# Performance work log

Measured on AMD Instinct MI355X. Metric: run time of the kernel, lower is better.

Reference implementation:

```python
import math
import jax, jax.numpy as jnp
import numpy as np

WS = 8      # window_size
NT = 16     # n_theta
NR = 8      # n_r
PD = 32     # polar_proj_dim


def _polar_grid():
    # Matches LocalPolarPrior._build_polar_grid: [NR, NT, 2] with (x, y) in [-1, 1]
    radius = jnp.linspace(0.0, 1.0, NR)
    theta = jnp.linspace(0.0, 2.0 * math.pi, NT + 1)[:-1]
    rr, tt = jnp.meshgrid(radius, theta, indexing='ij')
    return jnp.stack([rr * jnp.cos(tt), rr * jnp.sin(tt)], axis=-1)


def _bilinear_weights():
    # Precompute flat gather indices + weights for F.grid_sample(mode='bilinear',
    # padding_mode='zeros', align_corners=True) on a fixed WSxWS input.
    g = _polar_grid()                                   # [NR, NT, 2]
    px = (g[..., 0] + 1.0) * 0.5 * (WS - 1)             # x -> pixel coords
    py = (g[..., 1] + 1.0) * 0.5 * (WS - 1)
    x0 = jnp.floor(px); y0 = jnp.floor(py)
    wx = px - x0; wy = py - y0
    xs = jnp.stack([x0, x0 + 1, x0, x0 + 1], axis=-1)   # [NR, NT, 4]
    ys = jnp.stack([y0, y0, y0 + 1, y0 + 1], axis=-1)
    ws = jnp.stack([(1 - wx) * (1 - wy), wx * (1 - wy),
                    (1 - wx) * wy, wx * wy], axis=-1)
    valid = (xs >= 0) & (xs < WS) & (ys >= 0) & (ys < WS)
    xi = jnp.clip(xs, 0, WS - 1).astype(jnp.int32)
    yi = jnp.clip(ys, 0, WS - 1).astype(jnp.int32)
    idx = (yi * WS + xi).reshape(NR * NT, 4)            # flat [0, 64)
    wt = (ws * valid).reshape(NR * NT, 4).astype(jnp.float32)
    return idx, wt


def setup_inputs() -> dict:
    key = jax.random.key(0)
    k1, k2, k3 = jax.random.split(key, 3)
    x = jax.random.normal(k1, (8, 96, 384, 384), jnp.float32)
    W_proj = jax.random.normal(k2, (PD, 96), jnp.float32) * 0.1
    b_proj = jax.random.normal(k3, (PD,), jnp.float32) * 0.1
    return {"x": x, "W_proj": W_proj, "b_proj": b_proj}


def reference(x, W_proj, b_proj):
    B, C, H, W = x.shape
    hg, wg = H // WS, W // WS
    # 1x1 conv projection
    feat = jnp.einsum('bchw,oc->bohw', x, W_proj) + b_proj[None, :, None, None]
    # window partition -> [B*hg*wg, PD, WS, WS]
    win = (feat.reshape(B, PD, hg, WS, wg, WS)
               .transpose(0, 2, 4, 1, 3, 5)
               .reshape(B * hg * wg, PD, WS, WS))
    # per-window orthonormal FFT2, shift, log-magnitude
    spec = jnp.fft.fftshift(jnp.fft.fft2(win, norm='ortho'), axes=(-2, -1))
    mag = jnp.log1p(jnp.abs(spec))                      # [N, PD, WS, WS]
    # fixed bilinear polar resample (data-independent weights)
    idx, wt = _bilinear_weights()                       # [NR*NT, 4]
    magf = mag.reshape(-1, PD, WS * WS)
    samp = magf[:, :, idx]                              # [N, PD, NR*NT, 4]
    polar = (samp * wt).sum(-1).reshape(-1, PD, NR, NT)
    # direction distribution per window
    logits = polar.mean(axis=(1, 2))                    # [N, NT]
    dist = jax.nn.softmax(logits, axis=-1)
    d_local = dist.reshape(B, hg, wg, NT).transpose(0, 3, 1, 2)
    entropy = -(d_local * jnp.log(jnp.clip(d_local, 1e-8))).sum(axis=1, keepdims=True)
    confidence = jnp.clip(1.0 - entropy / math.log(NT), 0.0, 1.0)
    return d_local.astype(x.dtype), confidence.astype(x.dtype)
```

## Files before the change

### kernel.cpp

```cpp
#include <hip/hip_runtime.h>
#include <hip/hip_bf16.h>
#include <math.h>

#define NT 16
#define NR 8
#define PD 32
#define HG 48
#define WG 48
#define NB 8
#define CH 96
#define HW 384
#define XHW (HW * HW)
#define S8 0.70710678118654752f

typedef short short8 __attribute__((ext_vector_type(8)));
typedef float f32x4 __attribute__((ext_vector_type(4)));

static __device__ const float CT16[16] = {
    1.0f, 0.9238795325112867f, 0.7071067811865476f, 0.3826834323650898f,
    0.0f, -0.3826834323650898f, -0.7071067811865476f, -0.9238795325112867f,
    -1.0f, -0.9238795325112867f, -0.7071067811865476f, -0.3826834323650898f,
    0.0f, 0.3826834323650898f, 0.7071067811865476f, 0.9238795325112867f};
static __device__ const float ST16[16] = {
    0.0f, 0.3826834323650898f, 0.7071067811865476f, 0.9238795325112867f,
    1.0f, 0.9238795325112867f, 0.7071067811865476f, 0.3826834323650898f,
    0.0f, -0.3826834323650898f, -0.7071067811865476f, -0.9238795325112867f,
    -1.0f, -0.9238795325112867f, -0.7071067811865476f, -0.3826834323650898f};

static __device__ __forceinline__ unsigned short f2bf(float f) {
  unsigned int u = __float_as_uint(f);
  u = u + 0x7fffu + ((u >> 16) & 1u);
  return (unsigned short)(u >> 16);
}
static __device__ __forceinline__ unsigned int pk2bf(float a, float b) {
  union { __hip_bfloat162 h; unsigned int u; } c;
  c.h = __float22bfloat162_rn(make_float2(a, b));
  return c.u;
}
static __device__ __forceinline__ float bf2f_lo(unsigned int v) {
  return __uint_as_float(v << 16);
}
static __device__ __forceinline__ float bf2f_hi(unsigned int v) {
  return __uint_as_float(v & 0xffff0000u);
}

#define MAGR(x_) log1pf(0.125f * fabsf(x_))
#define MAGC(re_, im_) log1pf(0.125f * sqrtf((re_) * (re_) + (im_) * (im_)))

__global__ void lpp_setup(const float* __restrict__ Wp,
                          unsigned short* __restrict__ ws) {
  int gt = blockIdx.x * 256 + threadIdx.x;
  if (gt < 384) {
    int f = gt >> 6, l = gt & 63;
    int ks = f >> 1, nt = f & 1;
    int n = nt * 16 + (l & 15);
    int kbase = ks * 32 + (l >> 4) * 8;
    for (int jj = 0; jj < 8; ++jj)
      ws[(f * 64 + l) * 8 + jj] = f2bf(Wp[n * CH + kbase + jj]);
  }
  if (gt >= 1024 && gt < 2048) {
    int q = gt - 1024;
    int j = q >> 4, t = q & 15;
    float g = 0.f;
    for (int r = 0; r < 8; ++r) {
      float rad = (float)r / 7.0f;
      float px = (rad * CT16[t] + 1.0f) * 3.5f;
      float py = (rad * ST16[t] + 1.0f) * 3.5f;
      float xf = floorf(px), yf = floorf(py);
      float wx = px - xf, wy = py - yf;
      int ix = (int)xf, iy = (int)yf;
      int xi0 = min(max(ix, 0), 7), xi1 = min(max(ix + 1, 0), 7);
      int yi0 = min(max(iy, 0), 7), yi1 = min(max(iy + 1, 0), 7);
      bool vx0 = (ix >= 0) && (ix < 8), vx1 = (ix + 1 >= 0) && (ix + 1 < 8);
      bool vy0 = (iy >= 0) && (iy < 8), vy1 = (iy + 1 >= 0) && (iy + 1 < 8);
      float w0 = (vx0 && vy0) ? (1.f - wx) * (1.f - wy) : 0.f;
      float w1 = (vx1 && vy0) ? wx * (1.f - wy) : 0.f;
      float w2 = (vx0 && vy1) ? (1.f - wx) * wy : 0.f;
      float w3 = (vx1 && vy1) ? wx * wy : 0.f;
      if (yi0 * 8 + xi0 == j) g += w0;
      if (yi0 * 8 + xi1 == j) g += w1;
      if (yi1 * 8 + xi0 == j) g += w2;
      if (yi1 * 8 + xi1 == j) g += w3;
    }
    int f = j >> 5, kc = (j >> 3) & 3, jj = j & 7;
    int l = (kc << 4) | t;
    ws[3072 + (f * 64 + l) * 8 + jj] = f2bf(g);
  }
}

__global__ __launch_bounds__(256, 4) void lpp_main(
    const float* __restrict__ x, const float* __restrict__ bp,
    const unsigned short* __restrict__ ws, float* __restrict__ out) {
  __shared__ short8 ldsX[2048];
  __shared__ float obuf[144];
  unsigned int* ldsU = (unsigned int*)ldsX;

  const int tid = threadIdx.x;
  const int lane = tid & 63;
  const int wave = tid >> 6;
  const int gid = blockIdx.x;
  const int wxg = gid % 6;
  const int hy = (gid / 6) % HG;
  const int b = gid / (6 * HG);
  const short8* wsV = (const short8*)ws;

  f32x4 acc[8][2];
#pragma unroll
  for (int m = 0; m < 8; ++m) {
    acc[m][0] = (f32x4){0.f, 0.f, 0.f, 0.f};
    acc[m][1] = (f32x4){0.f, 0.f, 0.f, 0.f};
  }

  const size_t xcb = (size_t)b * CH * XHW;
  const int kcA = lane >> 4;
  for (int ks = 0; ks < 3; ++ks) {
    if (ks) __syncthreads();
#pragma unroll
    for (int g2 = 0; g2 < 2; ++g2) {
      int id = tid + 256 * g2;
      int kc = id >> 7;
      int p0 = (id & 127) << 2;
      int row = (p0 >> 3) & 7;
      int gcol = wxg * 64 + ((p0 >> 6) << 3) + (p0 & 7);
      const float* xp = x + xcb + (size_t)(ks * 32 + kc * 8) * XHW +
                        (size_t)(hy * 8 + row) * HW + gcol;
      float q[8][4];
#pragma unroll
      for (int jj = 0; jj < 8; ++jj) {
        float4 v = *(const float4*)(xp + (size_t)jj * XHW);
        q[jj][0] = v.x; q[jj][1] = v.y; q[jj][2] = v.z; q[jj][3] = v.w;
      }
      int z = (p0 >> 3) & 7;
      int base3 = kc * 512 + (p0 & ~7);
#pragma unroll
      for (int i = 0; i < 4; ++i) {
        union { unsigned int u[4]; short8 v; } pk;
#pragma unroll
        for (int k2 = 0; k2 < 4; ++k2)
          pk.u[k2] = pk2bf(q[2 * k2][i], q[2 * k2 + 1][i]);
        int u = base3 | ((((p0 & 4) | i)) ^ z);
        ldsX[u] = pk.v;
      }
    }
    __syncthreads();
    short8 b0 = wsV[(ks * 2 + 0) * 64 + lane];
    short8 b1 = wsV[(ks * 2 + 1) * 64 + lane];
    int prow = wave * 128 + (lane & 15);
#pragma unroll
    for (int m = 0; m < 8; ++m) {
      int p = prow + m * 16;
      int s = kcA * 512 + p;
      short8 a = ldsX[s ^ ((p >> 3) & 7)];
      acc[m][0] = __builtin_amdgcn_mfma_f32_16x16x32_bf16(a, b0, acc[m][0], 0, 0, 0);
      acc[m][1] = __builtin_amdgcn_mfma_f32_16x16x32_bf16(a, b1, acc[m][1], 0, 0, 0);
    }
  }
  __syncthreads();

  {
    const float bias0 = bp[lane & 15];
    const float bias1 = bp[16 + (lane & 15)];
    int jb = (lane >> 4) << 2;
#pragma unroll
    for (int m = 0; m < 8; ++m) {
      int win = 2 * wave + (m >> 2);
      int j0 = ((m & 3) << 4) + jb;
#pragma unroll
      for (int nt = 0; nt < 2; ++nt) {
        int p = win * 32 + nt * 16 + (lane & 15);
        float bs = nt ? bias1 : bias0;
        int sh = (p & 15) << 1;
        int dwb = p * 32;
        unsigned int w0 = pk2bf(acc[m][nt][0] + bs, acc[m][nt][1] + bs);
        unsigned int w1 = pk2bf(acc[m][nt][2] + bs, acc[m][nt][3] + bs);
        ldsU[dwb + ((j0 >> 1) ^ sh)] = w0;
        ldsU[dwb + (((j0 >> 1) + 1) ^ sh)] = w1;
      }
    }
  }
  __syncthreads();

  {
    const int p = tid;
    const int sh = (p & 15) << 1;
    const int dwb = p * 32;
    float rr[8][8];
#pragma unroll
    for (int k = 0; k < 8; ++k) {
      float v[8];
#pragma unroll
      for (int i = 0; i < 4; ++i) {
        unsigned int u = ldsU[dwb + ((k * 4 + i) ^ sh)];
        v[2 * i] = bf2f_lo(u);
        v[2 * i + 1] = bf2f_hi(u);
      }
      float a0 = v[0] + v[4], a1 = v[0] - v[4], a2 = v[2] + v[6], a3 = v[2] - v[6];
      float b0 = v[1] + v[5], b1 = v[1] - v[5], b2 = v[3] + v[7], b3 = v[3] - v[7];
      float e0 = a0 + a2, e2 = a0 - a2, o0 = b0 + b2, o2 = b0 - b2;
      float t1 = S8 * (b1 - b3), t2 = S8 * (b1 + b3);
      rr[k][0] = e0 + o0; rr[k][1] = e0 - o0;
      rr[k][2] = a1 + t1; rr[k][3] = -a3 - t2;
      rr[k][4] = e2;      rr[k][5] = -o2;
      rr[k][6] = a1 - t1; rr[k][7] = a3 - t2;
    }
    float mg0[5], mg4[5], mg1[8], mg2[8], mg3[8];
#define REALCOL(SLOT, OUT)                                                    \
  {                                                                           \
    float a0 = rr[0][SLOT] + rr[4][SLOT], a1 = rr[0][SLOT] - rr[4][SLOT];     \
    float a2 = rr[2][SLOT] + rr[6][SLOT], a3 = rr[2][SLOT] - rr[6][SLOT];     \
    float b0 = rr[1][SLOT] + rr[5][SLOT], b1 = rr[1][SLOT] - rr[5][SLOT];     \
    float b2 = rr[3][SLOT] + rr[7][SLOT], b3 = rr[3][SLOT] - rr[7][SLOT];     \
    float e0 = a0 + a2, e2 = a0 - a2, o0 = b0 + b2, o2 = b0 - b2;             \
    float t1 = S8 * (b1 - b3), t2 = S8 * (b1 + b3);                           \
    OUT[0] = MAGR(e0 + o0); OUT[4] = MAGR(e0 - o0);                           \
    OUT[1] = MAGC(a1 + t1, -a3 - t2);                                         \
    OUT[2] = MAGC(e2, -o2);                                                   \
    OUT[3] = MAGC(a1 - t1, a3 - t2);                                          \
  }
#define CPLXCOL(SR, SI, OUT)                                                  \
  {                                                                           \
    float t0r = rr[0][SR] + rr[4][SR], t0i = rr[0][SI] + rr[4][SI];           \
    float t1r = rr[0][SR] - rr[4][SR], t1i = rr[0][SI] - rr[4][SI];           \
    float t2r = rr[2][SR] + rr[6][SR], t2i = rr[2][SI] + rr[6][SI];           \
    float t3r = rr[2][SR] - rr[6][SR], t3i = rr[2][SI] - rr[6][SI];           \
    float E0r = t0r + t2r, E0i = t0i + t2i, E2r = t0r - t2r, E2i = t0i - t2i; \
    float E1r = t1r + t3i, E1i = t1i - t3r, E3r = t1r - t3i, E3i = t1i + t3r; \
    float u0r = rr[1][SR] + rr[5][SR], u0i = rr[1][SI] + rr[5][SI];           \
    float u1r = rr[1][SR] - rr[5][SR], u1i = rr[1][SI] - rr[5][SI];           \
    float u2r = rr[3][SR] + rr[7][SR], u2i = rr[3][SI] + rr[7][SI];           \
    float u3r = rr[3][SR] - rr[7][SR], u3i = rr[3][SI] - rr[7][SI];           \
    float O0r = u0r + u2r, O0i = u0i + u2i, O2r = u0r - u2r, O2i = u0i - u2i; \
    float O1r = u1r + u3i, O1i = u1i - u3r, O3r = u1r - u3i, O3i = u1i + u3r; \
    float W1r = S8 * (O1r + O1i), W1i = S8 * (O1i - O1r);                     \
    float W2r = O2i, W2i = -O2r;                                              \
    float W3r = S8 * (O3i - O3r), W3i = -S8 * (O3r + O3i);                    \
    OUT[0] = MAGC(E0r + O0r, E0i + O0i); OUT[4] = MAGC(E0r - O0r, E0i - O0i); \
    OUT[1] = MAGC(E1r + W1r, E1i + W1i); OUT[5] = MAGC(E1r - W1r, E1i - W1i); \
    OUT[2] = MAGC(E2r + W2r, E2i + W2i); OUT[6] = MAGC(E2r - W2r, E2i - W2i); \
    OUT[3] = MAGC(E3r + W3r, E3i + W3i); OUT[7] = MAGC(E3r - W3r, E3i - W3i); \
  }
    REALCOL(0, mg0)
    REALCOL(1, mg4)
    CPLXCOL(2, 3, mg1)
    CPLXCOL(4, 5, mg2)
    CPLXCOL(6, 7, mg3)
    const int pb8 = p * 8, p7 = p & 7;
#pragma unroll
    for (int up = 0; up < 8; ++up) {
      union { unsigned short h[8]; short8 v; } pk;
#pragma unroll
      for (int vp = 0; vp < 8; ++vp) {
        const int u = (up + 4) & 7, vx = (vp + 4) & 7;
        float m;
        if (vx == 0)      m = mg0[(u <= 4) ? u : (8 - u)];
        else if (vx == 4) m = mg4[(u <= 4) ? u : (8 - u)];
        else if (vx == 1) m = mg1[u];
        else if (vx == 2) m = mg2[u];
        else if (vx == 3) m = mg3[u];
        else { const int uu = (8 - u) & 7;
               m = (vx == 5) ? mg3[uu] : (vx == 6) ? mg2[uu] : mg1[uu]; }
        pk.h[vp] = f2bf(m);
      }
      ldsX[pb8 + (up ^ p7)] = pk.v;
    }
  }
  __syncthreads();

  {
    short8 gf0 = wsV[384 + lane];
    short8 gf1 = wsV[448 + lane];
    f32x4 ag[4];
#pragma unroll
    for (int pt = 0; pt < 4; ++pt) {
      int prow = (wave * 4 + pt) * 16 + (lane & 15);
      int p7 = prow & 7, pb = prow * 8;
      short8 a0 = ldsX[pb + (kcA ^ p7)];
      short8 a1 = ldsX[pb + ((kcA + 4) ^ p7)];
      f32x4 zf = (f32x4){0.f, 0.f, 0.f, 0.f};
      zf = __builtin_amdgcn_mfma_f32_16x16x32_bf16(a0, gf0, zf, 0, 0, 0);
      zf = __builtin_amdgcn_mfma_f32_16x16x32_bf16(a1, gf1, zf, 0, 0, 0);
      ag[pt] = zf;
    }
    float s0 = ag[0][0] + ag[0][1] + ag[0][2] + ag[0][3] +
               ag[1][0] + ag[1][1] + ag[1][2] + ag[1][3];
    float s1 = ag[2][0] + ag[2][1] + ag[2][2] + ag[2][3] +
               ag[3][0] + ag[3][1] + ag[3][2] + ag[3][3];
    s0 += __shfl_xor(s0, 16); s0 += __shfl_xor(s0, 32);
    s1 += __shfl_xor(s1, 16); s1 += __shfl_xor(s1, 32);
    float l0 = s0 * (1.0f / 256.0f), l1 = s1 * (1.0f / 256.0f);
    float m0 = l0, m1 = l1;
#pragma unroll
    for (int mk = 1; mk < 16; mk <<= 1) {
      m0 = fmaxf(m0, __shfl_xor(m0, mk));
      m1 = fmaxf(m1, __shfl_xor(m1, mk));
    }
    float e0 = expf(l0 - m0), e1 = expf(l1 - m1);
    float ss0 = e0, ss1 = e1;
#pragma unroll
    for (int mk = 1; mk < 16; mk <<= 1) {
      ss0 += __shfl_xor(ss0, mk);
      ss1 += __shfl_xor(ss1, mk);
    }
    float d0 = e0 / ss0, d1 = e1 / ss1;
    float h0 = -d0 * logf(fmaxf(d0, 1e-8f));
    float h1 = -d1 * logf(fmaxf(d1, 1e-8f));
#pragma unroll
    for (int mk = 1; mk < 16; mk <<= 1) {
      h0 += __shfl_xor(h0, mk);
      h1 += __shfl_xor(h1, mk);
    }
    float c0 = fminf(fmaxf(1.f - h0 * (1.0f / 2.7725887222397811f), 0.f), 1.f);
    float c1 = fminf(fmaxf(1.f - h1 * (1.0f / 2.7725887222397811f), 0.f), 1.f);
    if (lane < 16) {
      obuf[wave * 32 + lane] = d0;
      obuf[wave * 32 + 16 + lane] = d1;
    }
    if (lane == 0) {
      obuf[128 + wave * 2] = c0;
      obuf[128 + wave * 2 + 1] = c1;
    }
  }
  __syncthreads();

  if (tid < 128) {
    int t = tid >> 3, win = tid & 7;
    int wx = wxg * 8 + win;
    out[((size_t)(b * NT + t) * HG + hy) * WG + wx] = obuf[win * 16 + t];
  } else if (tid < 136) {
    int win = tid - 128;
    int wx = wxg * 8 + win;
    out[(size_t)NB * NT * HG * WG + ((size_t)b * HG + hy) * WG + wx] =
        obuf[128 + win];
  }
}

extern "C" void kernel_launch(void* const* d_in, const int* in_sizes, int n_in,
                              void* d_out, int out_size, void* d_ws,
                              size_t ws_size, hipStream_t stream) {
  (void)in_sizes; (void)n_in; (void)ws_size; (void)out_size;
  const float* x = (const float*)d_in[0];
  const float* Wp = (const float*)d_in[1];
  const float* bp = (const float*)d_in[2];
  unsigned short* ws = (unsigned short*)d_ws;
  float* out = (float*)d_out;
  lpp_setup<<<8, 256, 0, stream>>>(Wp, ws);
  lpp_main<<<NB * HG * 6, 256, 0, stream>>>(x, bp, ws, out);
}
```

Measured before the change: 135.4 us.

## Load MFMA A-operands directly from global, skipping LDS staging of input

Replaces the per-K-step cooperative float4 load into swizzled LDS plus barriers with per-lane scalar global loads that feed MFMA A-fragments directly. Loads are software double-buffered across 24 steps, and all B fragments are hoisted into registers. The pixel-to-accumulator mapping changes, so the epilogue index mapping is rewritten to match. This removes LDS writes and reads and three barriers, but trades coalesced float4 loads for scalar strided loads and raises register pressure.

```diff
diff --git a/kernel.cpp b/kernel.cpp
--- a/kernel.cpp
+++ b/kernel.cpp
@@ -103,6 +103,7 @@
   const int hy = (gid / 6) % HG;
   const int b = gid / (6 * HG);
   const short8* wsV = (const short8*)ws;
+  const int kcA = lane >> 4;
 
   f32x4 acc[8][2];
 #pragma unroll
@@ -111,60 +112,48 @@
     acc[m][1] = (f32x4){0.f, 0.f, 0.f, 0.f};
   }
 
-  const size_t xcb = (size_t)b * CH * XHW;
-  const int kcA = lane >> 4;
-  for (int ks = 0; ks < 3; ++ks) {
-    if (ks) __syncthreads();
-#pragma unroll
-    for (int g2 = 0; g2 < 2; ++g2) {
-      int id = tid + 256 * g2;
-      int kc = id >> 7;
-      int p0 = (id & 127) << 2;
-      int row = (p0 >> 3) & 7;
-      int gcol = wxg * 64 + ((p0 >> 6) << 3) + (p0 & 7);
-      const float* xp = x + xcb + (size_t)(ks * 32 + kc * 8) * XHW +
-                        (size_t)(hy * 8 + row) * HW + gcol;
-      float q[8][4];
-#pragma unroll
-      for (int jj = 0; jj < 8; ++jj) {
-        float4 v = *(const float4*)(xp + (size_t)jj * XHW);
-        q[jj][0] = v.x; q[jj][1] = v.y; q[jj][2] = v.z; q[jj][3] = v.w;
-      }
-      int z = (p0 >> 3) & 7;
-      int base3 = kc * 512 + (p0 & ~7);
-#pragma unroll
-      for (int i = 0; i < 4; ++i) {
-        union { unsigned int u[4]; short8 v; } pk;
-#pragma unroll
-        for (int k2 = 0; k2 < 4; ++k2)
-          pk.u[k2] = pk2bf(q[2 * k2][i], q[2 * k2 + 1][i]);
-        int u = base3 | ((((p0 & 4) | i)) ^ z);
-        ldsX[u] = pk.v;
-      }
-    }
-    __syncthreads();
-    short8 b0 = wsV[(ks * 2 + 0) * 64 + lane];
-    short8 b1 = wsV[(ks * 2 + 1) * 64 + lane];
-    int prow = wave * 128 + (lane & 15);
-#pragma unroll
-    for (int m = 0; m < 8; ++m) {
-      int p = prow + m * 16;
-      int s = kcA * 512 + p;
-      short8 a = ldsX[s ^ ((p >> 3) & 7)];
-      acc[m][0] = __builtin_amdgcn_mfma_f32_16x16x32_bf16(a, b0, acc[m][0], 0, 0, 0);
-      acc[m][1] = __builtin_amdgcn_mfma_f32_16x16x32_bf16(a, b1, acc[m][1], 0, 0, 0);
-    }
-  }
-  __syncthreads();
+  short8 bfr[6];
+#pragma unroll
+  for (int f = 0; f < 6; ++f) bfr[f] = wsV[f * 64 + lane];
+
+  const int pw = wave * 128 + (lane & 15);
+  const float* tb = x + (size_t)b * CH * XHW + (size_t)(hy * 8) * HW +
+                    wxg * 64 + (size_t)(kcA * 8) * XHW;
+
+  float lv[2][8];
+#define LOADSTEP(DST, S)                                                     \
+  {                                                                          \
+    int px_ = pw + ((S) & 7) * 16;                                           \
+    int pxo_ = (px_ >> 6) * HW + (px_ & 63);                                 \
+    _Pragma("unroll") for (int j = 0; j < 8; ++j)                            \
+        DST[j] = tb[(size_t)(((S) >> 3) * 32 + j) * XHW + pxo_];             \
+  }
+
+  LOADSTEP(lv[0], 0)
+#pragma unroll
+  for (int s = 0; s < 24; ++s) {
+    if (s + 1 < 24) LOADSTEP(lv[(s + 1) & 1], s + 1)
+    union { unsigned int u[4]; short8 v; } pk;
+    pk.u[0] = pk2bf(lv[s & 1][0], lv[s & 1][1]);
+    pk.u[1] = pk2bf(lv[s & 1][2], lv[s & 1][3]);
+    pk.u[2] = pk2bf(lv[s & 1][4], lv[s & 1][5]);
+    pk.u[3] = pk2bf(lv[s & 1][6], lv[s & 1][7]);
+    acc[s & 7][0] = __builtin_amdgcn_mfma_f32_16x16x32_bf16(
+        pk.v, bfr[(s >> 3) * 2 + 0], acc[s & 7][0], 0, 0, 0);
+    acc[s & 7][1] = __builtin_amdgcn_mfma_f32_16x16x32_bf16(
+        pk.v, bfr[(s >> 3) * 2 + 1], acc[s & 7][1], 0, 0, 0);
+  }
 
   {
     const float bias0 = bp[lane & 15];
     const float bias1 = bp[16 + (lane & 15)];
-    int jb = (lane >> 4) << 2;
+    const int r_ = 2 * wave;
+    const int c0 = ((lane >> 4) & 1) << 2;
+    const int wb = (lane >> 5) & 1;
 #pragma unroll
     for (int m = 0; m < 8; ++m) {
-      int win = 2 * wave + (m >> 2);
-      int j0 = ((m & 3) << 4) + jb;
+      int win = (2 * m + wb) & 7;
+      int j0 = (r_ + (m >> 2)) * 8 + c0;
 #pragma unroll
       for (int nt = 0; nt < 2; ++nt) {
         int p = win * 32 + nt * 16 + (lane & 15);
```

Result: no change. 137.7 us (+1.8%).
